# Optimization experiments

Measured on AMD Instinct MI355X. Metric: run time of the kernel, lower is better.

Reference implementation:

```python
import jax, jax.numpy as jnp
import numpy as np

V, E, H, T, B = 30000, 300, 300, 22, 4096

def setup_inputs() -> dict:
    key = jax.random.key(0)
    ks = jax.random.split(key, 10)
    cap = jax.random.randint(ks[0], (B, T), 0, V)
    cap_len = jax.random.randint(ks[1], (B,), 1, T + 1)  # valid lengths in [1, T]
    embed = jax.random.uniform(ks[2], (V, E), jnp.float32, -0.1, 0.1)
    s_ih = 1.0 / np.sqrt(H)
    W_ih = jax.random.uniform(ks[3], (4 * H, E), jnp.float32, -s_ih, s_ih)
    W_hh = jax.random.uniform(ks[4], (4 * H, H), jnp.float32, -s_ih, s_ih)
    b_ih = jax.random.uniform(ks[5], (4 * H,), jnp.float32, -s_ih, s_ih)
    b_hh = jax.random.uniform(ks[6], (4 * H,), jnp.float32, -s_ih, s_ih)
    v_wn = jax.random.normal(ks[7], (2, H), jnp.float32) * 0.05
    g_wn = jnp.linalg.norm(v_wn, axis=1)  # torch weight_norm init: g = ||v||
    b_cls = jnp.zeros((2,), jnp.float32)
    return {"cap": cap, "cap_len": cap_len, "embed": embed, "W_ih": W_ih,
            "W_hh": W_hh, "b_ih": b_ih, "b_hh": b_hh, "v_wn": v_wn,
            "g_wn": g_wn, "b_cls": b_cls}

def reference(cap, cap_len, embed, W_ih, W_hh, b_ih, b_hh, v_wn, g_wn, b_cls):
    Bn, Tn = cap.shape
    emb = embed[cap]                      # [B,T,E] embedding gather
    h0 = jnp.zeros((Bn, H), emb.dtype)
    c0 = jnp.zeros((Bn, H), emb.dtype)

    def step(carry, x_t):                 # x_t: [B,E]
        h, c = carry
        gates = x_t @ W_ih.T + b_ih + h @ W_hh.T + b_hh  # [B,4H]
        i, f, g, o = jnp.split(gates, 4, axis=-1)
        i = jax.nn.sigmoid(i); f = jax.nn.sigmoid(f); o = jax.nn.sigmoid(o)
        c = f * c + i * jnp.tanh(g)
        h = o * jnp.tanh(c)
        return (h, c), h

    _, hs = jax.lax.scan(step, (h0, c0), jnp.swapaxes(emb, 0, 1))  # hs: [T,B,H]
    hs = jnp.swapaxes(hs, 0, 1)                                    # [B,T,H]
    last = hs[jnp.arange(Bn), cap_len - 1]                         # [B,H] length-indexed gather
    # weight-normed linear head (dropout is identity at eval)
    W = g_wn[:, None] * v_wn / jnp.linalg.norm(v_wn, axis=1, keepdims=True)
    return last @ W.T + b_cls                                      # [B,2]
```

## Files before the change

kernel.cpp:

```cpp
#include <hip/hip_runtime.h>
#include <hip/hip_fp16.h>


#define TT 22
#define STEPS 22
#define NB 19
#define NGRP 8
#define GROWS 512
#define NWG (NB * NGRP)
#define NTHR 512
#define XSTR 608
#define WLS 616
#define BROWS 4096
#define BUFELT ((size_t)BROWS * XSTR)
#define SROWS 27

typedef _Float16 f16;
typedef _Float16 f16x8 __attribute__((ext_vector_type(8)));
typedef float    f32x4 __attribute__((ext_vector_type(4)));

__device__ __forceinline__ float sigm(float x) { return 1.0f / (1.0f + __expf(-x)); }
__device__ __forceinline__ float tanh_f(float x) {
    float ax = fabsf(x);
    float e = __expf(-2.0f * ax);
    return copysignf((1.0f - e) / (1.0f + e), x);
}
__device__ __forceinline__ f16x8 pack8(float4 a, float4 b) {
    f16x8 v;
    v[0] = (f16)a.x; v[1] = (f16)a.y; v[2] = (f16)a.z; v[3] = (f16)a.w;
    v[4] = (f16)b.x; v[5] = (f16)b.y; v[6] = (f16)b.z; v[7] = (f16)b.w;
    return v;
}

__global__ __launch_bounds__(NTHR, 2)
void lstm_ws(const int* __restrict__ cap, const int* __restrict__ cap_len,
             const float* __restrict__ embed,
             const float* __restrict__ Wih, const float* __restrict__ Whh,
             const float* __restrict__ bih, const float* __restrict__ bhh,
             const float* __restrict__ v_wn, const float* __restrict__ g_wn,
             const float* __restrict__ b_cls,
             f16* __restrict__ bufs, int depth,
             unsigned* __restrict__ bar, float* __restrict__ out)
{
    __shared__ f16 Wl[64 * WLS];
    __shared__ int capS[SROWS][TT];
    __shared__ float scaleS[2];
    __shared__ unsigned idsS[NB];

    const int tid = threadIdx.x;
    const int b   = blockIdx.x;
    const int grp = b & 7;
    const int nb  = b >> 3;
    const int mrow0 = grp * GROWS;
    const int wv = tid >> 6, ln = tid & 63, c = ln & 15, kg = ln >> 4;
    const bool ahead2 = (depth >= 3);

    unsigned* flags = bar + grp * 1024;
    unsigned* ids   = bar + grp * 1024 + 768;

    if (tid == 0)
        (void)__hip_atomic_load(flags, __ATOMIC_ACQUIRE, __HIP_MEMORY_SCOPE_AGENT);

    unsigned xcc;
    asm volatile("s_getreg_b32 %0, hwreg(HW_REG_XCC_ID)" : "=s"(xcc));
    if (tid == 0)
        __hip_atomic_store(ids + nb, xcc + 1u, __ATOMIC_RELAXED,
                           __HIP_MEMORY_SCOPE_AGENT);

    auto slot = [&](int n) { return bufs + (size_t)(n % depth) * BUFELT; };

    for (int u = tid; u < 64 * 76; u += NTHR) {
        int col = u / 76, k8 = u - col * 76;
        int g = col >> 4, cc = col & 15;
        int jh0 = nb * 16 + cc;
        int j = g * 300 + jh0;
        f16x8 v;
        #pragma unroll
        for (int i = 0; i < 8; ++i) {
            int kk = k8 * 8 + i;
            float x = 0.f;
            if (jh0 < 300) {
                if (kk < 300)      x = Wih[(size_t)j * 300 + kk];
                else if (kk < 600) x = Whh[(size_t)j * 300 + (kk - 300)];
            }
            v[i] = (f16)x;
        }
        *(f16x8*)&Wl[col * WLS + k8 * 8] = v;
    }

    const int srow0 = nb * SROWS;
    const int nr = (GROWS - srow0) < SROWS ? (GROWS - srow0) : SROWS;
    for (int u = tid; u < SROWS * TT; u += NTHR) {
        int rl = u / TT, t = u - rl * TT;
        if (rl < nr) capS[rl][t] = cap[(size_t)(mrow0 + srow0 + rl) * TT + t];
    }
    if (tid < 2) {
        float s = 0.f;
        for (int k = 0; k < 300; ++k) { float v = v_wn[tid * 300 + k]; s += v * v; }
        scaleS[tid] = g_wn[tid] * rsqrtf(s);
    }
    __syncthreads();

    auto stage_x = [&](int t, f16* bufn) {
        for (int u = tid; u < nr * 38; u += NTHR) {
            int rl = u / 38, ch = u - rl * 38;
            int grow = mrow0 + srow0 + rl;
            const float* er = embed + (size_t)capS[rl][t] * 300;
            f16* dst = bufn + (size_t)grow * XSTR;
            int k0 = ch * 8;
            if (ch < 37) {
                float4 a = *(const float4*)(er + k0);
                float4 bb = *(const float4*)(er + k0 + 4);
                *(f16x8*)(dst + k0) = pack8(a, bb);
            } else {
                float4 a = *(const float4*)(er + 296);
                f16* d2 = dst + 296;
                d2[0] = (f16)a.x; d2[1] = (f16)a.y; d2[2] = (f16)a.z; d2[3] = (f16)a.w;
            }
        }
    };

    auto arrive = [&](unsigned ph, bool rel) {
        __syncthreads();
        if (tid == 0) {
            if (rel)
                __hip_atomic_store(flags + nb * 32, ph, __ATOMIC_RELEASE,
                                   __HIP_MEMORY_SCOPE_AGENT);
            else
                __hip_atomic_store(flags + nb * 32, ph, __ATOMIC_RELAXED,
                                   __HIP_MEMORY_SCOPE_AGENT);
        }
    };
    auto wait = [&](unsigned ph, bool fen) {
        if (tid < NB) {
            while (__hip_atomic_load(flags + tid * 32, __ATOMIC_RELAXED,
                                     __HIP_MEMORY_SCOPE_AGENT) < ph)
                __builtin_amdgcn_s_sleep(1);
        }
        if (fen)
            __builtin_amdgcn_fence(__ATOMIC_ACQUIRE, "agent");
        __syncthreads();
    };

    int aoff[4];
    #pragma unroll
    for (int m = 0; m < 4; ++m)
        aoff[m] = (mrow0 + wv * 64 + m * 16 + c) * XSTR + kg * 8;
    int bbase[4];
    #pragma unroll
    for (int g = 0; g < 4; ++g) bbase[g] = (g * 16 + c) * WLS + kg * 8;

    const int jh = nb * 16 + c;
    float bias[4];
    #pragma unroll
    for (int g = 0; g < 4; ++g) {
        float bv = 0.f;
        if (jh < 300) { int j = g * 300 + jh; bv = bih[j] + bhh[j]; }
        bias[g] = bv;
    }
    int lenr[4][4];
    #pragma unroll
    for (int m = 0; m < 4; ++m) {
        int rb = mrow0 + wv * 64 + m * 16 + kg * 4;
        #pragma unroll
        for (int rg = 0; rg < 4; ++rg) lenr[m][rg] = cap_len[rb + rg];
    }

    float cst[4][4] = {};
    float hreg[4][4] = {};
    f32x4 acc[4][4];

    auto xpart = [&](const f16* bufc) {
        #pragma unroll
        for (int kt = 0; kt < 9; ++kt) {
            f16x8 av[4];
            #pragma unroll
            for (int m = 0; m < 4; ++m)
                av[m] = *(const f16x8*)(bufc + aoff[m] + kt * 32);
            #pragma unroll
            for (int g = 0; g < 4; ++g) {
                f16x8 bv = *(const f16x8*)&Wl[bbase[g] + kt * 32];
                #pragma unroll
                for (int m = 0; m < 4; ++m)
                    acc[m][g] = __builtin_amdgcn_mfma_f32_16x16x32_f16(av[m], bv, acc[m][g], 0, 0, 0);
            }
        }
    };
    auto hpart = [&](const f16* bufc) {
        #pragma unroll
        for (int kt = 9; kt < 19; ++kt) {
            f16x8 av[4];
            #pragma unroll
            for (int m = 0; m < 4; ++m)
                av[m] = *(const f16x8*)(bufc + aoff[m] + kt * 32);
            #pragma unroll
            for (int g = 0; g < 4; ++g) {
                f16x8 bv = *(const f16x8*)&Wl[bbase[g] + kt * 32];
                #pragma unroll
                for (int m = 0; m < 4; ++m)
                    acc[m][g] = __builtin_amdgcn_mfma_f32_16x16x32_f16(av[m], bv, acc[m][g], 0, 0, 0);
            }
        }
    };

    stage_x(0, slot(0));
    if (ahead2) stage_x(1, slot(1));
    arrive(1, true);
    wait(1, true);

    if (tid < NB)
        idsS[tid] = __hip_atomic_load(ids + tid, __ATOMIC_RELAXED,
                                      __HIP_MEMORY_SCOPE_AGENT);
    __syncthreads();
    bool fastp = true;
    #pragma unroll 1
    for (int i = 1; i < NB; ++i) fastp = fastp && (idsS[i] == idsS[0]);

    #pragma unroll 1
    for (int t = 0; t < STEPS; ++t) {
        const f16* bufc = slot(t);
        #pragma unroll
        for (int m = 0; m < 4; ++m)
            #pragma unroll
            for (int g = 0; g < 4; ++g) {
                float bv = bias[g];
                f32x4 b4 = {bv, bv, bv, bv};
                acc[m][g] = b4;
            }

        bool reuse = (unsigned)(t + 1) >= (unsigned)depth;
        if (ahead2) {
            xpart(bufc);
            wait((unsigned)(t + 1), reuse);
        } else {
            wait((unsigned)(t + 1), reuse);
            xpart(bufc);
        }
        hpart(bufc);

        f16* bufn = slot(t + 1);
        #pragma unroll
        for (int m = 0; m < 4; ++m) {
            #pragma unroll
            for (int rg = 0; rg < 4; ++rg) {
                bool upd = (t < lenr[m][rg]);
                float iv = sigm(acc[m][0][rg]);
                float fv = sigm(acc[m][1][rg]);
                float gv = tanh_f(acc[m][2][rg]);
                float ov = sigm(acc[m][3][rg]);
                float cn = fv * cst[m][rg] + iv * gv;
                cn = upd ? cn : cst[m][rg];
                cst[m][rg] = cn;
                float hn = ov * tanh_f(cn);
                hreg[m][rg] = upd ? hn : hreg[m][rg];
            }
            if (jh < 300) {
                int rb = mrow0 + wv * 64 + m * 16 + kg * 4;
                #pragma unroll
                for (int rg = 0; rg < 4; ++rg)
                    bufn[(size_t)(rb + rg) * XSTR + 300 + jh] = (f16)hreg[m][rg];
            }
        }

        if (ahead2) { if (t + 2 < STEPS) stage_x(t + 2, slot(t + 2)); }
        else        { if (t + 1 < STEPS) stage_x(t + 1, slot(t + 1)); }
        arrive((unsigned)(t + 2), !fastp);
    }

    wait((unsigned)(STEPS + 1), true);

    const f16* hb = slot(STEPS);
    for (int u = tid; u < nr * 2; u += NTHR) {
        int rl = u >> 1, cls = u & 1;
        int grow = mrow0 + srow0 + rl;
        float sc = scaleS[cls];
        const float* vr = v_wn + cls * 300;
        const f16* hr = hb + (size_t)grow * XSTR + 300;
        float s = 0.f;
        #pragma unroll 4
        for (int k = 0; k < 300; ++k) s += vr[k] * (float)hr[k];
        out[(size_t)grow * 2 + cls] = sc * s + b_cls[cls];
    }
}

extern "C" void kernel_launch(void* const* d_in, const int* in_sizes, int n_in,
                              void* d_out, int out_size, void* d_ws, size_t ws_size,
                              hipStream_t stream) {
    const int*   cap     = (const int*)  d_in[0];
    const int*   cap_len = (const int*)  d_in[1];
    const float* embed   = (const float*)d_in[2];
    const float* W_ih    = (const float*)d_in[3];
    const float* W_hh    = (const float*)d_in[4];
    const float* b_ih    = (const float*)d_in[5];
    const float* b_hh    = (const float*)d_in[6];
    const float* v_wn    = (const float*)d_in[7];
    const float* g_wn    = (const float*)d_in[8];
    const float* b_cls   = (const float*)d_in[9];
    float* out = (float*)d_out;

    unsigned* bar = (unsigned*)d_ws;
    f16* bufs = (f16*)((char*)d_ws + 65536);
    size_t slot_bytes = BUFELT * sizeof(f16);
    int depth = (int)((ws_size > 65536 ? ws_size - 65536 : 0) / slot_bytes);
    if (depth > STEPS + 1) depth = STEPS + 1;
    if (depth < 2) depth = 2;

    hipMemsetAsync(bar, 0, 65536, stream);
    hipMemsetAsync(bufs, 0, slot_bytes, stream);

    lstm_ws<<<NWG, NTHR, 0, stream>>>(cap, cap_len, embed, W_ih, W_hh, b_ih, b_hh,
                                      v_wn, g_wn, b_cls, bufs, depth, bar, out);
}
```

Before: 431.7 us.

## Hoist input projection out of LSTM recurrence into batched precompute kernels

```diff
diff --git a/kernel.cpp b/kernel.cpp
--- a/kernel.cpp
+++ b/kernel.cpp
@@ -8,14 +8,9 @@
 #define NGRP 8
 #define GROWS 512
 #define NWG (NB * NGRP)
-#define NTHR 512
-#define XSTR 608
-#define WLS 616
-#define BROWS 4096
-#define BUFELT ((size_t)BROWS * XSTR)
-#define SROWS 27
 
 typedef _Float16 f16;
+typedef _Float16 f16x4 __attribute__((ext_vector_type(4)));
 typedef _Float16 f16x8 __attribute__((ext_vector_type(8)));
 typedef float    f32x4 __attribute__((ext_vector_type(4)));
 
@@ -32,15 +27,321 @@
     return v;
 }
 
-__global__ __launch_bounds__(NTHR, 2)
-void lstm_ws(const int* __restrict__ cap, const int* __restrict__ cap_len,
-             const float* __restrict__ embed,
-             const float* __restrict__ Wih, const float* __restrict__ Whh,
-             const float* __restrict__ bih, const float* __restrict__ bhh,
-             const float* __restrict__ v_wn, const float* __restrict__ g_wn,
-             const float* __restrict__ b_cls,
-             f16* __restrict__ bufs, int depth,
-             unsigned* __restrict__ bar, float* __restrict__ out)
+#define XK 320
+#define WXLS 328
+#define XBYTES   ((size_t)TT * 4096 * XK * 2)
+#define GXPER    ((size_t)TT * 64 * 512)
+#define GXBYTES  ((size_t)NWG * GXPER * 2)
+#define HBYTES   ((size_t)2 * 4096 * XK * 2)
+#define FLBYTES  ((size_t)65536)
+#define TIERA_BYTES (FLBYTES + XBYTES + GXBYTES + HBYTES)
+
+__global__ void stage_x_all(const int* __restrict__ cap,
+                            const float* __restrict__ embed,
+                            f16* __restrict__ xb)
+{
+    const unsigned NCH = TT * 4096u * 40u;
+    for (unsigned id = blockIdx.x * 256u + threadIdx.x; id < NCH;
+         id += gridDim.x * 256u) {
+        unsigned t  = id / (4096u * 40u);
+        unsigned r2 = id - t * 4096u * 40u;
+        unsigned row = r2 / 40u, k8 = r2 - row * 40u;
+        int tok = cap[row * TT + t];
+        const float* er = embed + (size_t)tok * 300;
+        f16* dst = xb + ((size_t)t * 4096 + row) * XK + k8 * 8;
+        unsigned k0 = k8 * 8;
+        f16x8 v;
+        if (k0 < 296) {
+            v = pack8(*(const float4*)(er + k0), *(const float4*)(er + k0 + 4));
+        } else if (k0 == 296) {
+            float4 a = *(const float4*)(er + 296);
+            v[0] = (f16)a.x; v[1] = (f16)a.y; v[2] = (f16)a.z; v[3] = (f16)a.w;
+            v[4] = v[5] = v[6] = v[7] = (f16)0.f;
+        } else {
+            #pragma unroll
+            for (int i = 0; i < 8; ++i) v[i] = (f16)0.f;
+        }
+        *(f16x8*)dst = v;
+    }
+}
+
+__global__ __launch_bounds__(1024, 1)
+void gx_pre(const float* __restrict__ Wih,
+            const float* __restrict__ bih, const float* __restrict__ bhh,
+            const f16* __restrict__ xb, f16* __restrict__ gxb)
+{
+    __shared__ f16 Wl[64 * WXLS];
+    const int tid = threadIdx.x, b = blockIdx.x;
+    const int grp = b & 7, nb = b >> 3;
+    const int mrow0 = grp * GROWS;
+    const int wv = tid >> 6, ln = tid & 63, c = ln & 15, kg = ln >> 4;
+
+    for (int u = tid; u < 64 * 41; u += 1024) {
+        int col = u / 41, k8 = u - col * 41;
+        int g = col >> 4, cc = col & 15;
+        int jh0 = nb * 16 + cc;
+        int j = g * 300 + jh0;
+        f16x8 v;
+        #pragma unroll
+        for (int i = 0; i < 8; ++i) {
+            int kk = k8 * 8 + i;
+            float x = (jh0 < 300 && kk < 300) ? Wih[(size_t)j * 300 + kk] : 0.f;
+            v[i] = (f16)x;
+        }
+        *(f16x8*)&Wl[col * WXLS + k8 * 8] = v;
+    }
+    __syncthreads();
+
+    const int jh = nb * 16 + c;
+    float bias[4];
+    #pragma unroll
+    for (int g = 0; g < 4; ++g)
+        bias[g] = (jh < 300) ? bih[g * 300 + jh] + bhh[g * 300 + jh] : 0.f;
+    int bbase[4];
+    #pragma unroll
+    for (int g = 0; g < 4; ++g) bbase[g] = (g * 16 + c) * WXLS + kg * 8;
+    size_t arow[2];
+    #pragma unroll
+    for (int m = 0; m < 2; ++m)
+        arow[m] = (size_t)(mrow0 + wv * 32 + m * 16 + c) * XK + kg * 8;
+
+    f16* gxw = gxb + (size_t)b * GXPER;
+
+    #pragma unroll 1
+    for (int t = 0; t < TT; ++t) {
+        f32x4 acc[2][4];
+        #pragma unroll
+        for (int m = 0; m < 2; ++m)
+            #pragma unroll
+            for (int g = 0; g < 4; ++g) {
+                float bv = bias[g];
+                f32x4 b4 = {bv, bv, bv, bv};
+                acc[m][g] = b4;
+            }
+        const f16* xt = xb + (size_t)t * 4096 * XK;
+        #pragma unroll
+        for (int kt = 0; kt < 10; ++kt) {
+            f16x8 av[2];
+            #pragma unroll
+            for (int m = 0; m < 2; ++m)
+                av[m] = *(const f16x8*)(xt + arow[m] + kt * 32);
+            #pragma unroll
+            for (int g = 0; g < 4; ++g) {
+                f16x8 bv = *(const f16x8*)&Wl[bbase[g] + kt * 32];
+                #pragma unroll
+                for (int m = 0; m < 2; ++m)
+                    acc[m][g] = __builtin_amdgcn_mfma_f32_16x16x32_f16(av[m], bv, acc[m][g], 0, 0, 0);
+            }
+        }
+        #pragma unroll
+        for (int m = 0; m < 2; ++m)
+            #pragma unroll
+            for (int g = 0; g < 4; ++g) {
+                f16x4 o;
+                #pragma unroll
+                for (int rg = 0; rg < 4; ++rg) o[rg] = (f16)acc[m][g][rg];
+                *(f16x4*)(gxw + ((size_t)(t * 64 + g * 16 + c) * 512
+                                 + wv * 32 + m * 16 + kg * 4)) = o;
+            }
+    }
+}
+
+#define SROWS 27
+
+__global__ __launch_bounds__(1024, 1)
+void lstm_rec(const int* __restrict__ cap_len,
+              const float* __restrict__ Whh,
+              const float* __restrict__ v_wn, const float* __restrict__ g_wn,
+              const float* __restrict__ b_cls,
+              const f16* __restrict__ gxb, f16* __restrict__ hbuf,
+              unsigned* __restrict__ bar, float* __restrict__ out)
+{
+    __shared__ f16 Wl[64 * WXLS];
+    __shared__ float scaleS[2];
+    __shared__ unsigned idsS[NB];
+
+    const int tid = threadIdx.x, b = blockIdx.x;
+    const int grp = b & 7, nb = b >> 3;
+    const int mrow0 = grp * GROWS;
+    const int wv = tid >> 6, ln = tid & 63, c = ln & 15, kg = ln >> 4;
+
+    unsigned* flags = bar + grp * 1024;
+    unsigned* ids   = bar + grp * 1024 + 768;
+
+    if (tid == 0)
+        (void)__hip_atomic_load(flags, __ATOMIC_ACQUIRE, __HIP_MEMORY_SCOPE_AGENT);
+    unsigned xcc;
+    asm volatile("s_getreg_b32 %0, hwreg(HW_REG_XCC_ID)" : "=s"(xcc));
+    if (tid == 0)
+        __hip_atomic_store(ids + nb, xcc + 1u, __ATOMIC_RELAXED,
+                           __HIP_MEMORY_SCOPE_AGENT);
+
+    for (int u = tid; u < 64 * 41; u += 1024) {
+        int col = u / 41, k8 = u - col * 41;
+        int g = col >> 4, cc = col & 15;
+        int jh0 = nb * 16 + cc;
+        int j = g * 300 + jh0;
+        f16x8 v;
+        #pragma unroll
+        for (int i = 0; i < 8; ++i) {
+            int kk = k8 * 8 + i;
+            float x = (jh0 < 300 && kk < 300) ? Whh[(size_t)j * 300 + kk] : 0.f;
+            v[i] = (f16)x;
+        }
+        *(f16x8*)&Wl[col * WXLS + k8 * 8] = v;
+    }
+    if (tid < 2) {
+        float s = 0.f;
+        for (int k = 0; k < 300; ++k) { float v = v_wn[tid * 300 + k]; s += v * v; }
+        scaleS[tid] = g_wn[tid] * rsqrtf(s);
+    }
+    __syncthreads();
+
+    auto arrive = [&](unsigned ph, bool rel) {
+        __syncthreads();
+        if (tid == 0) {
+            if (rel)
+                __hip_atomic_store(flags + nb * 32, ph, __ATOMIC_RELEASE,
+                                   __HIP_MEMORY_SCOPE_AGENT);
+            else
+                __hip_atomic_store(flags + nb * 32, ph, __ATOMIC_RELAXED,
+                                   __HIP_MEMORY_SCOPE_AGENT);
+        }
+    };
+    auto wait = [&](unsigned ph, bool fen) {
+        if (tid < NB) {
+            while (__hip_atomic_load(flags + tid * 32, __ATOMIC_RELAXED,
+                                     __HIP_MEMORY_SCOPE_AGENT) < ph)
+                __builtin_amdgcn_s_sleep(1);
+        }
+        if (fen)
+            __builtin_amdgcn_fence(__ATOMIC_ACQUIRE, "agent");
+        __syncthreads();
+    };
+
+    int bbase[4];
+    #pragma unroll
+    for (int g = 0; g < 4; ++g) bbase[g] = (g * 16 + c) * WXLS + kg * 8;
+    size_t aoff[2];
+    #pragma unroll
+    for (int m = 0; m < 2; ++m)
+        aoff[m] = (size_t)(mrow0 + wv * 32 + m * 16 + c) * XK + kg * 8;
+
+    const int jh = nb * 16 + c;
+    int lenr[2][4];
+    #pragma unroll
+    for (int m = 0; m < 2; ++m) {
+        int rb = mrow0 + wv * 32 + m * 16 + kg * 4;
+        #pragma unroll
+        for (int rg = 0; rg < 4; ++rg) lenr[m][rg] = cap_len[rb + rg];
+    }
+
+    const f16* gxr = gxb + (size_t)b * GXPER;
+    float cst[2][4] = {};
+    float hreg[2][4] = {};
+
+    arrive(1, true);
+    wait(1, true);
+
+    if (tid < NB)
+        idsS[tid] = __hip_atomic_load(ids + tid, __ATOMIC_RELAXED,
+                                      __HIP_MEMORY_SCOPE_AGENT);
+    __syncthreads();
+    bool fastp = true;
+    #pragma unroll 1
+    for (int i = 1; i < NB; ++i) fastp = fastp && (idsS[i] == idsS[0]);
+
+    #pragma unroll 1
+    for (int t = 0; t < STEPS; ++t) {
+        f32x4 acc[2][4];
+        #pragma unroll
+        for (int m = 0; m < 2; ++m)
+            #pragma unroll
+            for (int g = 0; g < 4; ++g) {
+                f16x4 gv = *(const f16x4*)(gxr + ((size_t)(t * 64 + g * 16 + c) * 512
+                                                  + wv * 32 + m * 16 + kg * 4));
+                #pragma unroll
+                for (int rg = 0; rg < 4; ++rg) acc[m][g][rg] = (float)gv[rg];
+            }
+
+        if (t > 0) {
+            wait((unsigned)(t + 1), true);
+            const f16* bufc = hbuf + (size_t)(t & 1) * 4096 * XK;
+            #pragma unroll
+            for (int kt = 0; kt < 10; ++kt) {
+                f16x8 av[2];
+                #pragma unroll
+                for (int m = 0; m < 2; ++m)
+                    av[m] = *(const f16x8*)(bufc + aoff[m] + kt * 32);
+                #pragma unroll
+                for (int g = 0; g < 4; ++g) {
+                    f16x8 bv = *(const f16x8*)&Wl[bbase[g] + kt * 32];
+                    #pragma unroll
+                    for (int m = 0; m < 2; ++m)
+                        acc[m][g] = __builtin_amdgcn_mfma_f32_16x16x32_f16(av[m], bv, acc[m][g], 0, 0, 0);
+                }
+            }
+        }
+
+        f16* bufn = hbuf + (size_t)((t + 1) & 1) * 4096 * XK;
+        #pragma unroll
+        for (int m = 0; m < 2; ++m) {
+            #pragma unroll
+            for (int rg = 0; rg < 4; ++rg) {
+                bool upd = (t < lenr[m][rg]);
+                float iv = sigm(acc[m][0][rg]);
+                float fv = sigm(acc[m][1][rg]);
+                float gv = tanh_f(acc[m][2][rg]);
+                float ov = sigm(acc[m][3][rg]);
+                float cn = fv * cst[m][rg] + iv * gv;
+                cn = upd ? cn : cst[m][rg];
+                cst[m][rg] = cn;
+                float hn = ov * tanh_f(cn);
+                hreg[m][rg] = upd ? hn : hreg[m][rg];
+            }
+            if (jh < 300) {
+                int rb = mrow0 + wv * 32 + m * 16 + kg * 4;
+                #pragma unroll
+                for (int rg = 0; rg < 4; ++rg)
+                    bufn[(size_t)(rb + rg) * XK + jh] = (f16)hreg[m][rg];
+            }
+        }
+        arrive((unsigned)(t + 2), !fastp);
+    }
+
+    wait((unsigned)(STEPS + 1), true);
+
+    const int srow0 = nb * SROWS;
+    const int nr = (GROWS - srow0) < SROWS ? (GROWS - srow0) : SROWS;
+    const f16* hb = hbuf + (size_t)(STEPS & 1) * 4096 * XK;
+    for (int u = tid; u < nr * 2; u += 1024) {
+        int rl = u >> 1, cls = u & 1;
+        int grow = mrow0 + srow0 + rl;
+        float sc = scaleS[cls];
+        const float* vr = v_wn + cls * 300;
+        const f16* hr = hb + (size_t)grow * XK;
+        float s = 0.f;
+        #pragma unroll 4
+        for (int k = 0; k < 300; ++k) s += vr[k] * (float)hr[k];
+        out[(size_t)grow * 2 + cls] = sc * s + b_cls[cls];
+    }
+}
+
+#define XSTR 608
+#define WLS 616
+#define BROWS 4096
+#define BUFELT ((size_t)BROWS * XSTR)
+#define NTHRC 512
+
+__global__ __launch_bounds__(NTHRC, 2)
+void lstm_ws_fb(const int* __restrict__ cap, const int* __restrict__ cap_len,
+                const float* __restrict__ embed,
+                const float* __restrict__ Wih, const float* __restrict__ Whh,
+                const float* __restrict__ bih, const float* __restrict__ bhh,
+                const float* __restrict__ v_wn, const float* __restrict__ g_wn,
+                const float* __restrict__ b_cls,
+                f16* __restrict__ bufs, int depth,
+                unsigned* __restrict__ bar, float* __restrict__ out)
 {
     __shared__ f16 Wl[64 * WLS];
     __shared__ int capS[SROWS][TT];
@@ -60,7 +361,6 @@
 
     if (tid == 0)
         (void)__hip_atomic_load(flags, __ATOMIC_ACQUIRE, __HIP_MEMORY_SCOPE_AGENT);
-
     unsigned xcc;
     asm volatile("s_getreg_b32 %0, hwreg(HW_REG_XCC_ID)" : "=s"(xcc));
     if (tid == 0)
@@ -69,7 +369,7 @@
 
     auto slot = [&](int n) { return bufs + (size_t)(n % depth) * BUFELT; };
 
-    for (int u = tid; u < 64 * 76; u += NTHR) {
+    for (int u = tid; u < 64 * 76; u += NTHRC) {
         int col = u / 76, k8 = u - col * 76;
         int g = col >> 4, cc = col & 15;
         int jh0 = nb * 16 + cc;
@@ -90,7 +390,7 @@
 
     const int srow0 = nb * SROWS;
     const int nr = (GROWS - srow0) < SROWS ? (GROWS - srow0) : SROWS;
-    for (int u = tid; u < SROWS * TT; u += NTHR) {
+    for (int u = tid; u < SROWS * TT; u += NTHRC) {
         int rl = u / TT, t = u - rl * TT;
         if (rl < nr) capS[rl][t] = cap[(size_t)(mrow0 + srow0 + rl) * TT + t];
     }
@@ -102,7 +402,7 @@
     __syncthreads();
 
     auto stage_x = [&](int t, f16* bufn) {
-        for (int u = tid; u < nr * 38; u += NTHR) {
+        for (int u = tid; u < nr * 38; u += NTHRC) {
             int rl = u / 38, ch = u - rl * 38;
             int grow = mrow0 + srow0 + rl;
             const float* er = embed + (size_t)capS[rl][t] * 300;
@@ -270,7 +570,7 @@
     wait((unsigned)(STEPS + 1), true);
 
     const f16* hb = slot(STEPS);
-    for (int u = tid; u < nr * 2; u += NTHR) {
+    for (int u = tid; u < nr * 2; u += NTHRC) {
         int rl = u >> 1, cls = u & 1;
         int grow = mrow0 + srow0 + rl;
         float sc = scaleS[cls];
@@ -298,16 +598,32 @@
     const float* b_cls   = (const float*)d_in[9];
     float* out = (float*)d_out;
 
-    unsigned* bar = (unsigned*)d_ws;
-    f16* bufs = (f16*)((char*)d_ws + 65536);
-    size_t slot_bytes = BUFELT * sizeof(f16);
-    int depth = (int)((ws_size > 65536 ? ws_size - 65536 : 0) / slot_bytes);
-    if (depth > STEPS + 1) depth = STEPS + 1;
-    if (depth < 2) depth = 2;
-
-    hipMemsetAsync(bar, 0, 65536, stream);
-    hipMemsetAsync(bufs, 0, slot_bytes, stream);
-
-    lstm_ws<<<NWG, NTHR, 0, stream>>>(cap, cap_len, embed, W_ih, W_hh, b_ih, b_hh,
-                                      v_wn, g_wn, b_cls, bufs, depth, bar, out);
+    if (ws_size >= TIERA_BYTES) {
+        unsigned* bar = (unsigned*)d_ws;
+        f16* xb   = (f16*)((char*)d_ws + FLBYTES);
+        f16* gxb  = (f16*)((char*)d_ws + FLBYTES + XBYTES);
+        f16* hbuf = (f16*)((char*)d_ws + FLBYTES + XBYTES + GXBYTES);
+
+        hipMemsetAsync(bar, 0, FLBYTES, stream);
+        hipMemsetAsync(hbuf, 0, HBYTES, stream);
+
+        stage_x_all<<<2048, 256, 0, stream>>>(cap, embed, xb);
+        gx_pre<<<NWG, 1024, 0, stream>>>(W_ih, b_ih, b_hh, xb, gxb);
+        lstm_rec<<<NWG, 1024, 0, stream>>>(cap_len, W_hh, v_wn, g_wn, b_cls,
+                                           gxb, hbuf, bar, out);
+    } else {
+        unsigned* bar = (unsigned*)d_ws;
+        f16* bufs = (f16*)((char*)d_ws + 65536);
+        size_t slot_bytes = BUFELT * sizeof(f16);
+        int depth = (int)((ws_size > 65536 ? ws_size - 65536 : 0) / slot_bytes);
+        if (depth > STEPS + 1) depth = STEPS + 1;
+        if (depth < 2) depth = 2;
+
+        hipMemsetAsync(bar, 0, 65536, stream);
+        hipMemsetAsync(bufs, 0, slot_bytes, stream);
+
+        lstm_ws_fb<<<NWG, NTHRC, 0, stream>>>(cap, cap_len, embed, W_ih, W_hh,
+                                              b_ih, b_hh, v_wn, g_wn, b_cls,
+                                              bufs, depth, bar, out);
+    }
 }
```

After: 431.4 us. No clear change (-0.1%).

## Tile activation buffers into MFMA-contiguous blocks and double waves per workgroup

Applied to the files above, without the earlier changes.

```diff
diff --git a/kernel.cpp b/kernel.cpp
--- a/kernel.cpp
+++ b/kernel.cpp
@@ -8,11 +8,10 @@
 #define NGRP 8
 #define GROWS 512
 #define NWG (NB * NGRP)
-#define NTHR 512
-#define XSTR 608
-#define WLS 616
-#define BROWS 4096
-#define BUFELT ((size_t)BROWS * XSTR)
+#define NTHR 1024
+#define KTOT 20
+#define WLS 680
+#define BUFELT ((size_t)256 * KTOT * 512)
 #define SROWS 27
 
 typedef _Float16 f16;
@@ -32,7 +31,7 @@
     return v;
 }
 
-__global__ __launch_bounds__(NTHR, 2)
+__global__ __launch_bounds__(NTHR, 4)
 void lstm_ws(const int* __restrict__ cap, const int* __restrict__ cap_len,
              const float* __restrict__ embed,
              const float* __restrict__ Wih, const float* __restrict__ Whh,
@@ -53,14 +52,12 @@
     const int nb  = b >> 3;
     const int mrow0 = grp * GROWS;
     const int wv = tid >> 6, ln = tid & 63, c = ln & 15, kg = ln >> 4;
-    const bool ahead2 = (depth >= 3);
 
     unsigned* flags = bar + grp * 1024;
     unsigned* ids   = bar + grp * 1024 + 768;
 
     if (tid == 0)
         (void)__hip_atomic_load(flags, __ATOMIC_ACQUIRE, __HIP_MEMORY_SCOPE_AGENT);
-
     unsigned xcc;
     asm volatile("s_getreg_b32 %0, hwreg(HW_REG_XCC_ID)" : "=s"(xcc));
     if (tid == 0)
@@ -69,8 +66,8 @@
 
     auto slot = [&](int n) { return bufs + (size_t)(n % depth) * BUFELT; };
 
-    for (int u = tid; u < 64 * 76; u += NTHR) {
-        int col = u / 76, k8 = u - col * 76;
+    for (int u = tid; u < 64 * 80; u += NTHR) {
+        int col = u / 80, k8 = u - col * 80;
         int g = col >> 4, cc = col & 15;
         int jh0 = nb * 16 + cc;
         int j = g * 300 + jh0;
@@ -80,8 +77,8 @@
             int kk = k8 * 8 + i;
             float x = 0.f;
             if (jh0 < 300) {
-                if (kk < 300)      x = Wih[(size_t)j * 300 + kk];
-                else if (kk < 600) x = Whh[(size_t)j * 300 + (kk - 300)];
+                if (kk < 300)                   x = Wih[(size_t)j * 300 + kk];
+                else if (kk >= 320 && kk < 620) x = Whh[(size_t)j * 300 + (kk - 320)];
             }
             v[i] = (f16)x;
         }
@@ -102,21 +99,25 @@
     __syncthreads();
 
     auto stage_x = [&](int t, f16* bufn) {
-        for (int u = tid; u < nr * 38; u += NTHR) {
-            int rl = u / 38, ch = u - rl * 38;
+        for (int u = tid; u < nr * 40; u += NTHR) {
+            int rl = u / 40, k8 = u - rl * 40;
             int grow = mrow0 + srow0 + rl;
             const float* er = embed + (size_t)capS[rl][t] * 300;
-            f16* dst = bufn + (size_t)grow * XSTR;
-            int k0 = ch * 8;
-            if (ch < 37) {
-                float4 a = *(const float4*)(er + k0);
-                float4 bb = *(const float4*)(er + k0 + 4);
-                *(f16x8*)(dst + k0) = pack8(a, bb);
+            int k0 = k8 * 8;
+            f16x8 v;
+            if (k0 < 296) {
+                v = pack8(*(const float4*)(er + k0), *(const float4*)(er + k0 + 4));
+            } else if (k0 == 296) {
+                float4 a = *(const float4*)(er + 296);
+                v[0] = (f16)a.x; v[1] = (f16)a.y; v[2] = (f16)a.z; v[3] = (f16)a.w;
+                v[4] = v[5] = v[6] = v[7] = (f16)0.f;
             } else {
-                float4 a = *(const float4*)(er + 296);
-                f16* d2 = dst + 296;
-                d2[0] = (f16)a.x; d2[1] = (f16)a.y; d2[2] = (f16)a.z; d2[3] = (f16)a.w;
-            }
+                #pragma unroll
+                for (int i = 0; i < 8; ++i) v[i] = (f16)0.f;
+            }
+            size_t off = ((size_t)((grow >> 4) * KTOT + (k8 >> 2))) * 512
+                         + (grow & 15) * 32 + (k8 & 3) * 8;
+            *(f16x8*)(bufn + off) = v;
         }
     };
 
@@ -142,10 +143,11 @@
         __syncthreads();
     };
 
-    int aoff[4];
+    size_t aoff[2];
     #pragma unroll
-    for (int m = 0; m < 4; ++m)
-        aoff[m] = (mrow0 + wv * 64 + m * 16 + c) * XSTR + kg * 8;
+    for (int m = 0; m < 2; ++m)
+        aoff[m] = (size_t)(((mrow0 >> 4) + wv * 2 + m) * KTOT) * 512
+                  + c * 32 + kg * 8;
     int bbase[4];
     #pragma unroll
     for (int g = 0; g < 4; ++g) bbase[g] = (g * 16 + c) * WLS + kg * 8;
@@ -158,51 +160,55 @@
         if (jh < 300) { int j = g * 300 + jh; bv = bih[j] + bhh[j]; }
         bias[g] = bv;
     }
-    int lenr[4][4];
+    int lenr[2][4];
     #pragma unroll
-    for (int m = 0; m < 4; ++m) {
-        int rb = mrow0 + wv * 64 + m * 16 + kg * 4;
+    for (int m = 0; m < 2; ++m) {
+        int rb = mrow0 + wv * 32 + m * 16 + kg * 4;
         #pragma unroll
         for (int rg = 0; rg < 4; ++rg) lenr[m][rg] = cap_len[rb + rg];
     }
-
-    float cst[4][4] = {};
-    float hreg[4][4] = {};
-    f32x4 acc[4][4];
+    const int hkt  = (320 + jh) >> 5;
+    const int hkgd = ((320 + jh) >> 3) & 3;
+    const int hel  = jh & 7;
+
+    float cst[2][4] = {};
+    float hreg[2][4] = {};
+    f32x4 acc[2][4];
 
     auto xpart = [&](const f16* bufc) {
         #pragma unroll
-        for (int kt = 0; kt < 9; ++kt) {
-            f16x8 av[4];
-            #pragma unroll
-            for (int m = 0; m < 4; ++m)
-                av[m] = *(const f16x8*)(bufc + aoff[m] + kt * 32);
+        for (int kt = 0; kt < 10; ++kt) {
+            f16x8 av[2];
+            #pragma unroll
+            for (int m = 0; m < 2; ++m)
+                av[m] = *(const f16x8*)(bufc + aoff[m] + kt * 512);
             #pragma unroll
             for (int g = 0; g < 4; ++g) {
                 f16x8 bv = *(const f16x8*)&Wl[bbase[g] + kt * 32];
                 #pragma unroll
-                for (int m = 0; m < 4; ++m)
+                for (int m = 0; m < 2; ++m)
                     acc[m][g] = __builtin_amdgcn_mfma_f32_16x16x32_f16(av[m], bv, acc[m][g], 0, 0, 0);
             }
         }
     };
     auto hpart = [&](const f16* bufc) {
         #pragma unroll
-        for (int kt = 9; kt < 19; ++kt) {
-            f16x8 av[4];
-            #pragma unroll
-            for (int m = 0; m < 4; ++m)
-                av[m] = *(const f16x8*)(bufc + aoff[m] + kt * 32);
+        for (int kt = 10; kt < KTOT; ++kt) {
+            f16x8 av[2];
+            #pragma unroll
+            for (int m = 0; m < 2; ++m)
+                av[m] = *(const f16x8*)(bufc + aoff[m] + kt * 512);
             #pragma unroll
             for (int g = 0; g < 4; ++g) {
                 f16x8 bv = *(const f16x8*)&Wl[bbase[g] + kt * 32];
                 #pragma unroll
-                for (int m = 0; m < 4; ++m)
+                for (int m = 0; m < 2; ++m)
                     acc[m][g] = __builtin_amdgcn_mfma_f32_16x16x32_f16(av[m], bv, acc[m][g], 0, 0, 0);
             }
         }
     };
 
+    const bool ahead2 = (depth >= 3);
     stage_x(0, slot(0));
     if (ahead2) stage_x(1, slot(1));
     arrive(1, true);
@@ -220,7 +226,7 @@
     for (int t = 0; t < STEPS; ++t) {
         const f16* bufc = slot(t);
         #pragma unroll
-        for (int m = 0; m < 4; ++m)
+        for (int m = 0; m < 2; ++m)
             #pragma unroll
             for (int g = 0; g < 4; ++g) {
                 float bv = bias[g];
@@ -240,7 +246,9 @@
 
         f16* bufn = slot(t + 1);
         #pragma unroll
-        for (int m = 0; m < 4; ++m) {
+        for (int m = 0; m < 2; ++m) {
+            int rtile = (mrow0 >> 4) + wv * 2 + m;
+            size_t hb = ((size_t)(rtile * KTOT + hkt)) * 512 + hkgd * 8 + hel;
             #pragma unroll
             for (int rg = 0; rg < 4; ++rg) {
                 bool upd = (t < lenr[m][rg]);
@@ -253,12 +261,8 @@
                 cst[m][rg] = cn;
                 float hn = ov * tanh_f(cn);
                 hreg[m][rg] = upd ? hn : hreg[m][rg];
-            }
-            if (jh < 300) {
-                int rb = mrow0 + wv * 64 + m * 16 + kg * 4;
-                #pragma unroll
-                for (int rg = 0; rg < 4; ++rg)
-                    bufn[(size_t)(rb + rg) * XSTR + 300 + jh] = (f16)hreg[m][rg];
+                f16 hv = (jh < 300) ? (f16)hreg[m][rg] : (f16)0.f;
+                bufn[hb + (size_t)(kg * 4 + rg) * 32] = hv;
             }
         }
 
@@ -275,10 +279,14 @@
         int grow = mrow0 + srow0 + rl;
         float sc = scaleS[cls];
         const float* vr = v_wn + cls * 300;
-        const f16* hr = hb + (size_t)grow * XSTR + 300;
+        size_t rbase = ((size_t)((grow >> 4) * KTOT)) * 512 + (grow & 15) * 32;
         float s = 0.f;
         #pragma unroll 4
-        for (int k = 0; k < 300; ++k) s += vr[k] * (float)hr[k];
+        for (int k = 0; k < 300; ++k) {
+            int k2 = 320 + k;
+            size_t off = rbase + (size_t)(k2 >> 5) * 512 + ((k2 >> 3) & 3) * 8 + (k2 & 7);
+            s += vr[k] * (float)hb[off];
+        }
         out[(size_t)grow * 2 + cls] = sc * s + b_cls[cls];
     }
 }
```

New measurement: 418.8 us. 3.0% less time.

## Split LSTM into producer blocks for input projection and recurrent consumer blocks

Applied to the files above, without the earlier changes.

```diff
diff --git a/kernel.cpp b/kernel.cpp
--- a/kernel.cpp
+++ b/kernel.cpp
@@ -5,17 +5,18 @@
 #define TT 22
 #define STEPS 22
 #define NB 19
-#define NGRP 8
-#define GROWS 512
-#define NWG (NB * NGRP)
+#define NHELP 11
+#define NWG 240
 #define NTHR 512
-#define XSTR 608
-#define WLS 616
-#define BROWS 4096
-#define BUFELT ((size_t)BROWS * XSTR)
+#define KT 10
 #define SROWS 27
+#define GD 4
+#define XD 5
+#define HSLOT ((size_t)256 * KT * 512)
+#define GXSLOT ((size_t)(8 * 19 * 4 * 32) * 256)
 
 typedef _Float16 f16;
+typedef _Float16 f16x4 __attribute__((ext_vector_type(4)));
 typedef _Float16 f16x8 __attribute__((ext_vector_type(8)));
 typedef float    f32x4 __attribute__((ext_vector_type(4)));
 
@@ -33,253 +34,361 @@
 }
 
 __global__ __launch_bounds__(NTHR, 2)
-void lstm_ws(const int* __restrict__ cap, const int* __restrict__ cap_len,
+void lstm_pc(const int* __restrict__ cap, const int* __restrict__ cap_len,
              const float* __restrict__ embed,
              const float* __restrict__ Wih, const float* __restrict__ Whh,
              const float* __restrict__ bih, const float* __restrict__ bhh,
              const float* __restrict__ v_wn, const float* __restrict__ g_wn,
              const float* __restrict__ b_cls,
-             f16* __restrict__ bufs, int depth,
-             unsigned* __restrict__ bar, float* __restrict__ out)
+             f16* __restrict__ gxb, f16* __restrict__ xb, f16* __restrict__ hbuf,
+             int HD, unsigned* __restrict__ bar, float* __restrict__ out)
 {
-    __shared__ f16 Wl[64 * WLS];
+    __shared__ f16 Wl[88 * 512];
     __shared__ int capS[SROWS][TT];
     __shared__ float scaleS[2];
-    __shared__ unsigned idsS[NB];
+    __shared__ unsigned idsS[20];
+    __shared__ int fastpS;
 
     const int tid = threadIdx.x;
-    const int b   = blockIdx.x;
+    const int b = blockIdx.x;
     const int grp = b & 7;
-    const int nb  = b >> 3;
-    const int mrow0 = grp * GROWS;
+    const int idx = b >> 3;
+    const int mrow0 = grp * 512;
     const int wv = tid >> 6, ln = tid & 63, c = ln & 15, kg = ln >> 4;
-    const bool ahead2 = (depth >= 3);
-
-    unsigned* flags = bar + grp * 1024;
-    unsigned* ids   = bar + grp * 1024 + 768;
-
-    if (tid == 0)
-        (void)__hip_atomic_load(flags, __ATOMIC_ACQUIRE, __HIP_MEMORY_SCOPE_AGENT);
-
+
+    unsigned* mfl = bar + grp * 1024;
+    unsigned* gfl = bar + grp * 1024 + 640;
+    unsigned* ids = bar + 8192 + grp * 32;
+
+    __builtin_amdgcn_fence(__ATOMIC_ACQUIRE, "agent");
     unsigned xcc;
     asm volatile("s_getreg_b32 %0, hwreg(HW_REG_XCC_ID)" : "=s"(xcc));
-    if (tid == 0)
-        __hip_atomic_store(ids + nb, xcc + 1u, __ATOMIC_RELAXED,
+    const unsigned myid = xcc + 1u;
+    if (tid == 0) {
+        __hip_atomic_store(ids + idx, myid, __ATOMIC_RELAXED,
                            __HIP_MEMORY_SCOPE_AGENT);
-
-    auto slot = [&](int n) { return bufs + (size_t)(n % depth) * BUFELT; };
-
-    for (int u = tid; u < 64 * 76; u += NTHR) {
-        int col = u / 76, k8 = u - col * 76;
-        int g = col >> 4, cc = col & 15;
-        int jh0 = nb * 16 + cc;
-        int j = g * 300 + jh0;
-        f16x8 v;
-        #pragma unroll
-        for (int i = 0; i < 8; ++i) {
-            int kk = k8 * 8 + i;
-            float x = 0.f;
-            if (jh0 < 300) {
-                if (kk < 300)      x = Wih[(size_t)j * 300 + kk];
-                else if (kk < 600) x = Whh[(size_t)j * 300 + (kk - 300)];
-            }
-            v[i] = (f16)x;
-        }
-        *(f16x8*)&Wl[col * WLS + k8 * 8] = v;
+        fastpS = 1;
     }
 
-    const int srow0 = nb * SROWS;
-    const int nr = (GROWS - srow0) < SROWS ? (GROWS - srow0) : SROWS;
-    for (int u = tid; u < SROWS * TT; u += NTHR) {
-        int rl = u / TT, t = u - rl * TT;
-        if (rl < nr) capS[rl][t] = cap[(size_t)(mrow0 + srow0 + rl) * TT + t];
-    }
-    if (tid < 2) {
-        float s = 0.f;
-        for (int k = 0; k < 300; ++k) { float v = v_wn[tid * 300 + k]; s += v * v; }
-        scaleS[tid] = g_wn[tid] * rsqrtf(s);
-    }
-    __syncthreads();
-
-    auto stage_x = [&](int t, f16* bufn) {
-        for (int u = tid; u < nr * 38; u += NTHR) {
-            int rl = u / 38, ch = u - rl * 38;
-            int grow = mrow0 + srow0 + rl;
-            const float* er = embed + (size_t)capS[rl][t] * 300;
-            f16* dst = bufn + (size_t)grow * XSTR;
-            int k0 = ch * 8;
-            if (ch < 37) {
-                float4 a = *(const float4*)(er + k0);
-                float4 bb = *(const float4*)(er + k0 + 4);
-                *(f16x8*)(dst + k0) = pack8(a, bb);
-            } else {
-                float4 a = *(const float4*)(er + 296);
-                f16* d2 = dst + 296;
-                d2[0] = (f16)a.x; d2[1] = (f16)a.y; d2[2] = (f16)a.z; d2[3] = (f16)a.w;
-            }
-        }
-    };
-
-    auto arrive = [&](unsigned ph, bool rel) {
-        __syncthreads();
-        if (tid == 0) {
-            if (rel)
-                __hip_atomic_store(flags + nb * 32, ph, __ATOMIC_RELEASE,
-                                   __HIP_MEMORY_SCOPE_AGENT);
-            else
-                __hip_atomic_store(flags + nb * 32, ph, __ATOMIC_RELAXED,
-                                   __HIP_MEMORY_SCOPE_AGENT);
-        }
-    };
-    auto wait = [&](unsigned ph, bool fen) {
+    auto waitM = [&](unsigned ph, bool fen) {
         if (tid < NB) {
-            while (__hip_atomic_load(flags + tid * 32, __ATOMIC_RELAXED,
+            while (__hip_atomic_load(mfl + tid * 32, __ATOMIC_RELAXED,
                                      __HIP_MEMORY_SCOPE_AGENT) < ph)
                 __builtin_amdgcn_s_sleep(1);
         }
-        if (fen)
-            __builtin_amdgcn_fence(__ATOMIC_ACQUIRE, "agent");
+        if (fen) __builtin_amdgcn_fence(__ATOMIC_ACQUIRE, "agent");
         __syncthreads();
     };
 
-    int aoff[4];
-    #pragma unroll
-    for (int m = 0; m < 4; ++m)
-        aoff[m] = (mrow0 + wv * 64 + m * 16 + c) * XSTR + kg * 8;
-    int bbase[4];
-    #pragma unroll
-    for (int g = 0; g < 4; ++g) bbase[g] = (g * 16 + c) * WLS + kg * 8;
-
-    const int jh = nb * 16 + c;
-    float bias[4];
-    #pragma unroll
-    for (int g = 0; g < 4; ++g) {
-        float bv = 0.f;
-        if (jh < 300) { int j = g * 300 + jh; bv = bih[j] + bhh[j]; }
-        bias[g] = bv;
-    }
-    int lenr[4][4];
-    #pragma unroll
-    for (int m = 0; m < 4; ++m) {
-        int rb = mrow0 + wv * 64 + m * 16 + kg * 4;
-        #pragma unroll
-        for (int rg = 0; rg < 4; ++rg) lenr[m][rg] = cap_len[rb + rg];
-    }
-
-    float cst[4][4] = {};
-    float hreg[4][4] = {};
-    f32x4 acc[4][4];
-
-    auto xpart = [&](const f16* bufc) {
-        #pragma unroll
-        for (int kt = 0; kt < 9; ++kt) {
-            f16x8 av[4];
-            #pragma unroll
-            for (int m = 0; m < 4; ++m)
-                av[m] = *(const f16x8*)(bufc + aoff[m] + kt * 32);
-            #pragma unroll
-            for (int g = 0; g < 4; ++g) {
-                f16x8 bv = *(const f16x8*)&Wl[bbase[g] + kt * 32];
-                #pragma unroll
-                for (int m = 0; m < 4; ++m)
-                    acc[m][g] = __builtin_amdgcn_mfma_f32_16x16x32_f16(av[m], bv, acc[m][g], 0, 0, 0);
-            }
-        }
-    };
-    auto hpart = [&](const f16* bufc) {
-        #pragma unroll
-        for (int kt = 9; kt < 19; ++kt) {
-            f16x8 av[4];
-            #pragma unroll
-            for (int m = 0; m < 4; ++m)
-                av[m] = *(const f16x8*)(bufc + aoff[m] + kt * 32);
-            #pragma unroll
-            for (int g = 0; g < 4; ++g) {
-                f16x8 bv = *(const f16x8*)&Wl[bbase[g] + kt * 32];
-                #pragma unroll
-                for (int m = 0; m < 4; ++m)
-                    acc[m][g] = __builtin_amdgcn_mfma_f32_16x16x32_f16(av[m], bv, acc[m][g], 0, 0, 0);
-            }
-        }
-    };
-
-    stage_x(0, slot(0));
-    if (ahead2) stage_x(1, slot(1));
-    arrive(1, true);
-    wait(1, true);
-
-    if (tid < NB)
-        idsS[tid] = __hip_atomic_load(ids + tid, __ATOMIC_RELAXED,
-                                      __HIP_MEMORY_SCOPE_AGENT);
-    __syncthreads();
-    bool fastp = true;
-    #pragma unroll 1
-    for (int i = 1; i < NB; ++i) fastp = fastp && (idsS[i] == idsS[0]);
-
-    #pragma unroll 1
-    for (int t = 0; t < STEPS; ++t) {
-        const f16* bufc = slot(t);
+    if (idx < NB) {
+        const int nb = idx;
+        const int owner = (nb <= 10) ? nb : nb - 11;
+        unsigned* ghp = gfl + owner * 32;
+
+        for (int u = tid; u < 40 * 64; u += NTHR) {
+            int f = u >> 6, l = u & 63;
+            int g = f / KT, kt = f - g * KT;
+            int jh0 = nb * 16 + (l & 15);
+            int kb = kt * 32 + (l >> 4) * 8;
+            f16x8 v;
+            #pragma unroll
+            for (int i = 0; i < 8; ++i) {
+                int kk = kb + i;
+                float x = (jh0 < 300 && kk < 300)
+                          ? Whh[(size_t)(g * 300 + jh0) * 300 + kk] : 0.f;
+                v[i] = (f16)x;
+            }
+            *(f16x8*)&Wl[(size_t)f * 512 + l * 8] = v;
+        }
+        const int srow0 = nb * SROWS;
+        const int nr = (512 - srow0) < SROWS ? (512 - srow0) : SROWS;
+        for (int u = tid; u < SROWS * TT; u += NTHR) {
+            int rl = u / TT, t = u - rl * TT;
+            if (rl < nr) capS[rl][t] = cap[(size_t)(mrow0 + srow0 + rl) * TT + t];
+        }
+        if (tid < 2) {
+            float s = 0.f;
+            for (int k = 0; k < 300; ++k) { float v = v_wn[tid * 300 + k]; s += v * v; }
+            scaleS[tid] = g_wn[tid] * rsqrtf(s);
+        }
+        __syncthreads();
+
+        auto stage_x = [&](int t) {
+            f16* bufn = xb + (size_t)(t % XD) * HSLOT;
+            for (int u = tid; u < nr * 40; u += NTHR) {
+                int rl = u / 40, k8 = u - rl * 40;
+                int grow = mrow0 + srow0 + rl;
+                const float* er = embed + (size_t)capS[rl][t] * 300;
+                int k0 = k8 * 8;
+                f16x8 v;
+                if (k0 < 296) {
+                    v = pack8(*(const float4*)(er + k0), *(const float4*)(er + k0 + 4));
+                } else if (k0 == 296) {
+                    float4 a = *(const float4*)(er + 296);
+                    v[0] = (f16)a.x; v[1] = (f16)a.y; v[2] = (f16)a.z; v[3] = (f16)a.w;
+                    v[4] = v[5] = v[6] = v[7] = (f16)0.f;
+                } else {
+                    #pragma unroll
+                    for (int i = 0; i < 8; ++i) v[i] = (f16)0.f;
+                }
+                size_t off = ((size_t)((grow >> 4) * KT + (k8 >> 2))) * 512
+                             + (grow & 15) * 32 + (k8 & 3) * 8;
+                *(f16x8*)(bufn + off) = v;
+            }
+        };
+
+        stage_x(0); stage_x(1); stage_x(2);
+        __syncthreads();
+        if (tid == 0)
+            __hip_atomic_store(mfl + nb * 32, 1u, __ATOMIC_RELEASE,
+                               __HIP_MEMORY_SCOPE_AGENT);
+        waitM(1, true);
+        if (tid < NB)
+            idsS[tid] = __hip_atomic_load(ids + tid, __ATOMIC_RELAXED,
+                                          __HIP_MEMORY_SCOPE_AGENT);
+        __syncthreads();
+
+        size_t aoff[4];
         #pragma unroll
         for (int m = 0; m < 4; ++m)
-            #pragma unroll
-            for (int g = 0; g < 4; ++g) {
-                float bv = bias[g];
-                f32x4 b4 = {bv, bv, bv, bv};
-                acc[m][g] = b4;
-            }
-
-        bool reuse = (unsigned)(t + 1) >= (unsigned)depth;
-        if (ahead2) {
-            xpart(bufc);
-            wait((unsigned)(t + 1), reuse);
-        } else {
-            wait((unsigned)(t + 1), reuse);
-            xpart(bufc);
-        }
-        hpart(bufc);
-
-        f16* bufn = slot(t + 1);
+            aoff[m] = ((size_t)((mrow0 >> 4) + wv * 4 + m) * KT) * 512 + c * 32 + kg * 8;
+        const int jh = nb * 16 + c;
+        int lenr[4][4];
         #pragma unroll
         for (int m = 0; m < 4; ++m) {
-            #pragma unroll
-            for (int rg = 0; rg < 4; ++rg) {
-                bool upd = (t < lenr[m][rg]);
-                float iv = sigm(acc[m][0][rg]);
-                float fv = sigm(acc[m][1][rg]);
-                float gv = tanh_f(acc[m][2][rg]);
-                float ov = sigm(acc[m][3][rg]);
-                float cn = fv * cst[m][rg] + iv * gv;
-                cn = upd ? cn : cst[m][rg];
-                cst[m][rg] = cn;
-                float hn = ov * tanh_f(cn);
-                hreg[m][rg] = upd ? hn : hreg[m][rg];
-            }
-            if (jh < 300) {
-                int rb = mrow0 + wv * 64 + m * 16 + kg * 4;
-                #pragma unroll
-                for (int rg = 0; rg < 4; ++rg)
-                    bufn[(size_t)(rb + rg) * XSTR + 300 + jh] = (f16)hreg[m][rg];
-            }
-        }
-
-        if (ahead2) { if (t + 2 < STEPS) stage_x(t + 2, slot(t + 2)); }
-        else        { if (t + 1 < STEPS) stage_x(t + 1, slot(t + 1)); }
-        arrive((unsigned)(t + 2), !fastp);
-    }
-
-    wait((unsigned)(STEPS + 1), true);
-
-    const f16* hb = slot(STEPS);
-    for (int u = tid; u < nr * 2; u += NTHR) {
-        int rl = u >> 1, cls = u & 1;
-        int grow = mrow0 + srow0 + rl;
-        float sc = scaleS[cls];
-        const float* vr = v_wn + cls * 300;
-        const f16* hr = hb + (size_t)grow * XSTR + 300;
-        float s = 0.f;
-        #pragma unroll 4
-        for (int k = 0; k < 300; ++k) s += vr[k] * (float)hr[k];
-        out[(size_t)grow * 2 + cls] = sc * s + b_cls[cls];
+            int rb = mrow0 + wv * 64 + m * 16 + kg * 4;
+            #pragma unroll
+            for (int rg = 0; rg < 4; ++rg) lenr[m][rg] = cap_len[rb + rg];
+        }
+        const int hkt = jh >> 5, hkgd = (jh >> 3) & 3, hel = jh & 7;
+        size_t gxoff[4][4];
+        #pragma unroll
+        for (int m = 0; m < 4; ++m)
+            #pragma unroll
+            for (int g = 0; g < 4; ++g)
+                gxoff[m][g] = ((((size_t)(grp * 19 + nb) * 4 + g) * 32
+                               + (wv * 4 + m)) * 256) + ln * 4;
+
+        float cst[4][4] = {};
+        float hreg[4][4] = {};
+        bool fastT = true;
+
+        #pragma unroll 1
+        for (int t = 0; t < STEPS; ++t) {
+            unsigned need = (unsigned)(t + 2);
+            while (__hip_atomic_load(ghp, __ATOMIC_RELAXED,
+                                     __HIP_MEMORY_SCOPE_AGENT) < need)
+                __builtin_amdgcn_s_sleep(1);
+            if (t == 0) {
+                __builtin_amdgcn_fence(__ATOMIC_ACQUIRE, "agent");
+                if (tid == 0) {
+                    idsS[19] = __hip_atomic_load(ids + NB + owner, __ATOMIC_RELAXED,
+                                                 __HIP_MEMORY_SCOPE_AGENT);
+                    bool f = true;
+                    for (int i = 0; i < 20; ++i) f = f && (idsS[i] == myid);
+                    fastpS = f ? 1 : 0;
+                }
+            } else if (!fastpS) {
+                __builtin_amdgcn_fence(__ATOMIC_ACQUIRE, "agent");
+            }
+
+            const f16* gxs = gxb + (size_t)(t % GD) * GXSLOT;
+            f32x4 acc[4][4];
+            #pragma unroll
+            for (int m = 0; m < 4; ++m)
+                #pragma unroll
+                for (int g = 0; g < 4; ++g) {
+                    f16x4 gv = __builtin_nontemporal_load(
+                                   (const f16x4*)(gxs + gxoff[m][g]));
+                    #pragma unroll
+                    for (int rg = 0; rg < 4; ++rg) acc[m][g][rg] = (float)gv[rg];
+                }
+
+            if (t > 0) {
+                bool fen = (t >= HD) || !fastpS;
+                waitM((unsigned)(t + 1), fen);
+                const f16* hs = hbuf + (size_t)(t % HD) * HSLOT;
+                #pragma unroll
+                for (int kt = 0; kt < KT; ++kt) {
+                    f16x8 av[4];
+                    #pragma unroll
+                    for (int m = 0; m < 4; ++m)
+                        av[m] = *(const f16x8*)(hs + aoff[m] + kt * 512);
+                    #pragma unroll
+                    for (int g = 0; g < 4; ++g) {
+                        f16x8 bv = *(const f16x8*)&Wl[(size_t)(g * KT + kt) * 512 + ln * 8];
+                        #pragma unroll
+                        for (int m = 0; m < 4; ++m)
+                            acc[m][g] = __builtin_amdgcn_mfma_f32_16x16x32_f16(av[m], bv, acc[m][g], 0, 0, 0);
+                    }
+                }
+            }
+
+            f16* hn = hbuf + (size_t)((t + 1) % HD) * HSLOT;
+            #pragma unroll
+            for (int m = 0; m < 4; ++m) {
+                int rtile = (mrow0 >> 4) + wv * 4 + m;
+                size_t hb0 = ((size_t)(rtile * KT + hkt)) * 512 + hkgd * 8 + hel;
+                #pragma unroll
+                for (int rg = 0; rg < 4; ++rg) {
+                    bool upd = (t < lenr[m][rg]);
+                    float iv = sigm(acc[m][0][rg]);
+                    float fv = sigm(acc[m][1][rg]);
+                    float gv = tanh_f(acc[m][2][rg]);
+                    float ov = sigm(acc[m][3][rg]);
+                    float cn = fv * cst[m][rg] + iv * gv;
+                    cn = upd ? cn : cst[m][rg];
+                    cst[m][rg] = cn;
+                    float hnv = ov * tanh_f(cn);
+                    hreg[m][rg] = upd ? hnv : hreg[m][rg];
+                    f16 hv = (jh < 300) ? (f16)hreg[m][rg] : (f16)0.f;
+                    hn[hb0 + (size_t)(kg * 4 + rg) * 32] = hv;
+                }
+            }
+
+            __syncthreads();
+            if (tid == 0) {
+                fastT = (fastpS != 0);
+                if (fastT)
+                    __hip_atomic_store(mfl + nb * 32, (unsigned)(t + 2),
+                                       __ATOMIC_RELAXED, __HIP_MEMORY_SCOPE_AGENT);
+                else
+                    __hip_atomic_store(mfl + nb * 32, (unsigned)(t + 2),
+                                       __ATOMIC_RELEASE, __HIP_MEMORY_SCOPE_AGENT);
+            }
+            if (t + 3 < STEPS) stage_x(t + 3);
+        }
+
+        waitM((unsigned)(STEPS + 1), true);
+
+        const f16* hs = hbuf + (size_t)(STEPS % HD) * HSLOT;
+        for (int u = tid; u < nr * 2; u += NTHR) {
+            int rl = u >> 1, cls = u & 1;
+            int grow = mrow0 + srow0 + rl;
+            float sc = scaleS[cls];
+            const float* vr = v_wn + cls * 300;
+            size_t rb = ((size_t)((grow >> 4) * KT)) * 512 + (grow & 15) * 32;
+            float s = 0.f;
+            #pragma unroll 4
+            for (int k = 0; k < 300; ++k) {
+                size_t off = rb + (size_t)(k >> 5) * 512 + ((k >> 3) & 3) * 8 + (k & 7);
+                s += vr[k] * (float)hs[off];
+            }
+            out[(size_t)grow * 2 + cls] = sc * s + b_cls[cls];
+        }
+    } else {
+        const int j = idx - NB;
+        const int nt = (j < 8) ? 2 : 1;
+        const int tiles[2] = { j, j + 11 };
+
+        for (int u = tid; u < nt * 40 * 64; u += NTHR) {
+            int f = u >> 6, l = u & 63;
+            int tl = f / 40, rest = f - tl * 40;
+            int g = rest / KT, kt = rest - g * KT;
+            int jh0 = tiles[tl] * 16 + (l & 15);
+            int kb = kt * 32 + (l >> 4) * 8;
+            f16x8 v;
+            #pragma unroll
+            for (int i = 0; i < 8; ++i) {
+                int kk = kb + i;
+                float x = (jh0 < 300 && kk < 300)
+                          ? Wih[(size_t)(g * 300 + jh0) * 300 + kk] : 0.f;
+                v[i] = (f16)x;
+            }
+            *(f16x8*)&Wl[(size_t)f * 512 + l * 8] = v;
+        }
+        float biasH[2][4];
+        #pragma unroll
+        for (int tl = 0; tl < 2; ++tl)
+            #pragma unroll
+            for (int g = 0; g < 4; ++g) {
+                int jh0 = tiles[tl] * 16 + c;
+                biasH[tl][g] = (tl < nt && jh0 < 300)
+                               ? bih[g * 300 + jh0] + bhh[g * 300 + jh0] : 0.f;
+            }
+        size_t xoff[4];
+        #pragma unroll
+        for (int m = 0; m < 4; ++m)
+            xoff[m] = ((size_t)((mrow0 >> 4) + wv * 4 + m) * KT) * 512 + c * 32 + kg * 8;
+        __syncthreads();
+
+        bool fastH = true;
+        #pragma unroll 1
+        for (int tw = 0; tw < STEPS; ++tw) {
+            unsigned need = (tw < 1) ? 1u : (unsigned)tw;
+            waitM(need, tw == 0 || !fastH);
+            if (tw == 0) {
+                if (tid < NB)
+                    idsS[tid] = __hip_atomic_load(ids + tid, __ATOMIC_RELAXED,
+                                                  __HIP_MEMORY_SCOPE_AGENT);
+                __syncthreads();
+                fastH = true;
+                for (int i = 0; i < NB; ++i) fastH = fastH && (idsS[i] == myid);
+            }
+
+            const f16* xs = xb + (size_t)(tw % XD) * HSLOT;
+            f16* gxs = gxb + (size_t)(tw % GD) * GXSLOT;
+
+            f32x4 acc[4][2][4];
+            #pragma unroll
+            for (int m = 0; m < 4; ++m)
+                #pragma unroll
+                for (int tl = 0; tl < 2; ++tl)
+                    #pragma unroll
+                    for (int g = 0; g < 4; ++g) {
+                        float bv = biasH[tl][g];
+                        f32x4 b4 = {bv, bv, bv, bv};
+                        acc[m][tl][g] = b4;
+                    }
+
+            #pragma unroll
+            for (int kt = 0; kt < KT; ++kt) {
+                f16x8 av[4];
+                #pragma unroll
+                for (int m = 0; m < 4; ++m)
+                    av[m] = __builtin_nontemporal_load(
+                                (const f16x8*)(xs + xoff[m] + kt * 512));
+                #pragma unroll
+                for (int tl = 0; tl < 2; ++tl) {
+                    if (tl < nt) {
+                        #pragma unroll
+                        for (int g = 0; g < 4; ++g) {
+                            f16x8 bv = *(const f16x8*)&Wl[(size_t)((tl * 4 + g) * KT + kt) * 512 + ln * 8];
+                            #pragma unroll
+                            for (int m = 0; m < 4; ++m)
+                                acc[m][tl][g] = __builtin_amdgcn_mfma_f32_16x16x32_f16(av[m], bv, acc[m][tl][g], 0, 0, 0);
+                        }
+                    }
+                }
+            }
+
+            #pragma unroll
+            for (int m = 0; m < 4; ++m)
+                #pragma unroll
+                for (int tl = 0; tl < 2; ++tl) {
+                    if (tl < nt) {
+                        #pragma unroll
+                        for (int g = 0; g < 4; ++g) {
+                            f16x4 o;
+                            #pragma unroll
+                            for (int rg = 0; rg < 4; ++rg) o[rg] = (f16)acc[m][tl][g][rg];
+                            size_t gi = ((((size_t)(grp * 19 + tiles[tl]) * 4 + g) * 32
+                                          + (wv * 4 + m)) * 256) + ln * 4;
+                            *(f16x4*)(gxs + gi) = o;
+                        }
+                    }
+                }
+
+            __syncthreads();
+            if (tid == 0) {
+                if (tw == 0 || !fastH)
+                    __hip_atomic_store(gfl + j * 32, (unsigned)(tw + 2),
+                                       __ATOMIC_RELEASE, __HIP_MEMORY_SCOPE_AGENT);
+                else
+                    __hip_atomic_store(gfl + j * 32, (unsigned)(tw + 2),
+                                       __ATOMIC_RELAXED, __HIP_MEMORY_SCOPE_AGENT);
+            }
+        }
     }
 }
 
@@ -299,15 +408,21 @@
     float* out = (float*)d_out;
 
     unsigned* bar = (unsigned*)d_ws;
-    f16* bufs = (f16*)((char*)d_ws + 65536);
-    size_t slot_bytes = BUFELT * sizeof(f16);
-    int depth = (int)((ws_size > 65536 ? ws_size - 65536 : 0) / slot_bytes);
-    if (depth > STEPS + 1) depth = STEPS + 1;
-    if (depth < 2) depth = 2;
+    f16* gxb  = (f16*)((char*)d_ws + 65536);
+    f16* xb   = gxb + GD * GXSLOT;
+    f16* hbuf = xb + XD * HSLOT;
+
+    size_t fixed = 65536 + (GD * GXSLOT + XD * HSLOT) * 2;
+    int HD = 2;
+    if (ws_size > fixed) {
+        size_t avail = (ws_size - fixed) / (HSLOT * 2);
+        HD = (int)(avail > 23 ? 23 : avail);
+        if (HD < 2) HD = 2;
+    }
 
     hipMemsetAsync(bar, 0, 65536, stream);
-    hipMemsetAsync(bufs, 0, slot_bytes, stream);
-
-    lstm_ws<<<NWG, NTHR, 0, stream>>>(cap, cap_len, embed, W_ih, W_hh, b_ih, b_hh,
-                                      v_wn, g_wn, b_cls, bufs, depth, bar, out);
+
+    lstm_pc<<<NWG, NTHR, 0, stream>>>(cap, cap_len, embed, W_ih, W_hh,
+                                      b_ih, b_hh, v_wn, g_wn, b_cls,
+                                      gxb, xb, hbuf, HD, bar, out);
 }
```

After: 400.4 us. 1.08x faster.
